# Kernel tuning notes

Hardware: AMD Instinct MI355X
Metric: run time of the kernel (lower is better)

## Reference

```python
import jax, jax.numpy as jnp
import numpy as np

B, S, HID = 1, 2048, 2048   # batch, block_size, hidden_dim
H, D = 16, 128              # num_heads, head_dim
WORLD_SIZE = 4
LOCAL_BLOCK_IDX = 3         # last rank: all kv blocks are causally visible


def setup_inputs() -> dict:
    key = jax.random.key(0)
    ks = jax.random.split(key, 5)
    w = lambda k: jax.random.normal(k, (H * D, HID), dtype=jnp.float32) * 0.02
    return {
        "hidden_states": jax.random.normal(ks[0], (B, S, HID), dtype=jnp.float32),
        "q_w": w(ks[1]), "q_b": jnp.zeros((H * D,), jnp.float32),
        "k_w": w(ks[2]), "k_b": jnp.zeros((H * D,), jnp.float32),
        "v_w": w(ks[3]), "v_b": jnp.zeros((H * D,), jnp.float32),
        "o_w": jax.random.normal(ks[4], (HID, H * D), dtype=jnp.float32) * 0.02,
        "o_b": jnp.zeros((HID,), jnp.float32),
        "world_size": WORLD_SIZE,
        "local_block_idx": LOCAL_BLOCK_IDX,
    }


def reference(hidden_states, q_w, q_b, k_w, k_b, v_w, v_b, o_w, o_b,
              world_size, local_block_idx):
    Bsz, Sq, _ = hidden_states.shape

    def proj(w, b):  # (B,S,HID) -> (B,H,S,D)
        return (hidden_states @ w.T + b).reshape(Bsz, Sq, H, D).transpose(0, 2, 1, 3)

    q, k, v = proj(q_w, q_b), proj(k_w, k_b), proj(v_w, v_b)
    scale = D ** -0.5

    # ring_send_recv is a local copy, so K/V are identical every ring step;
    # only the causal masking differs (triu mask on the diagonal block step).
    scores_base = jnp.einsum('bhqd,bhkd->bhqk', q, k) * scale
    tri = jnp.triu(jnp.ones((Sq, Sq), bool), k=1)
    scores_diag = jnp.where(tri, -jnp.inf, scores_base)

    out = jnp.zeros((Bsz, H, Sq, D), hidden_states.dtype)
    mx = jnp.full((Bsz, H, Sq, 1), -jnp.inf, hidden_states.dtype)
    se = jnp.zeros((Bsz, H, Sq, 1), hidden_states.dtype)

    for step in range(world_size):  # small fixed ring loop
        kv_idx = (local_block_idx - step) % world_size
        scores = scores_diag if kv_idx == local_block_idx else scores_base
        # OnlineSoftmax.update (faithful, including block-wise normalization)
        bm = scores.max(axis=-1, keepdims=True)
        nm = jnp.maximum(mx, bm)
        old_s = jnp.exp(mx - nm)
        new_s = jnp.exp(bm - nm)
        be = jnp.exp(scores - bm)
        bs = be.sum(axis=-1, keepdims=True)
        se = se * old_s + bs * new_s
        aw = be / (bs + 1e-8)
        bo = jnp.einsum('bhqk,bhkd->bhqd', aw, v)
        out = out * old_s + bo * new_s
        mx = nm

    out = out / (se + 1e-8)  # OnlineSoftmax.finalize
    out = out.transpose(0, 2, 1, 3).reshape(Bsz, Sq, H * D)
    return out @ o_w.T + o_b
```

## Files before the change

### kernel.cpp

```cpp
#include <hip/hip_runtime.h>
#include <hip/hip_bf16.h>
#include <stdint.h>
#include <stddef.h>


typedef __attribute__((ext_vector_type(8))) short bf16x8;
typedef __attribute__((ext_vector_type(4))) float f32x4;

#define MFMA_BF16(a, b, c) __builtin_amdgcn_mfma_f32_16x16x32_bf16((a), (b), (c), 0, 0, 0)

__device__ __forceinline__ void load16_lds(const void* g, void* l) {
  __builtin_amdgcn_global_load_lds((const __attribute__((address_space(1))) void*)g,
                                   (__attribute__((address_space(3))) void*)l,
                                   16, 0, 0);
}

__device__ __forceinline__ unsigned short f2bf(float x) {
  union { __hip_bfloat16 b; unsigned short u; } cv;
  cv.b = __float2bfloat16(x);
  return cv.u;
}

__global__ __launch_bounds__(256) void cvt_all(
    const float4* __restrict__ s0, const float4* __restrict__ s1,
    const float4* __restrict__ s2, const float4* __restrict__ s3,
    const float4* __restrict__ s4,
    ushort4* __restrict__ d0, ushort4* __restrict__ d1,
    ushort4* __restrict__ d2, ushort4* __restrict__ d3,
    ushort4* __restrict__ d4) {
  const int seg = blockIdx.x >> 12;
  const int i = ((blockIdx.x & 4095) << 8) + threadIdx.x;
  const float4* s = seg == 0 ? s0 : seg == 1 ? s1 : seg == 2 ? s2 : seg == 3 ? s3 : s4;
  ushort4* d = seg == 0 ? d0 : seg == 1 ? d1 : seg == 2 ? d2 : seg == 3 ? d3 : d4;
  float4 v = s[i];
  ushort4 o;
  o.x = f2bf(v.x); o.y = f2bf(v.y); o.z = f2bf(v.z); o.w = f2bf(v.w);
  d[i] = o;
}

__global__ __launch_bounds__(256) void gemm_qkv(
    const unsigned short* __restrict__ A, const unsigned short* __restrict__ Bt,
    const float* __restrict__ qb, const float* __restrict__ kb,
    const float* __restrict__ vb,
    unsigned short* __restrict__ Qo, unsigned short* __restrict__ Ko,
    unsigned short* __restrict__ Vt) {
  __shared__ __align__(16) unsigned short sA[128 * 64];
  __shared__ __align__(16) unsigned short sB[128 * 64];
  const int tid = threadIdx.x;
  const int wave = tid >> 6, lane = tid & 63;
  const int quad = lane >> 4, l16 = lane & 15;
  const int wr = wave >> 1, wc = wave & 1;
  const int m0 = blockIdx.y << 7, n0 = blockIdx.x << 7;

  f32x4 acc[4][4] = {};

  for (int k0 = 0; k0 < 2048; k0 += 64) {
    __syncthreads();
#pragma unroll
    for (int t = 0; t < 4; t++) {
      const int i = t * 4 + wave;
      const int idx = i * 64 + lane;
      const int row = idx >> 3;
      const int c = (idx & 7) ^ (row & 7);
      load16_lds(A + (size_t)(m0 + row) * 2048 + k0 + c * 8, &sA[i * 512]);
      load16_lds(Bt + (size_t)(n0 + row) * 2048 + k0 + c * 8, &sB[i * 512]);
    }
    __syncthreads();
#pragma unroll
    for (int ks = 0; ks < 2; ks++) {
      bf16x8 af[4], bfr[4];
#pragma unroll
      for (int i = 0; i < 4; i++) {
        const int cs = ((ks * 4 + quad) ^ (l16 & 7)) << 3;
        af[i] = *(const bf16x8*)&sA[(wr * 64 + i * 16 + l16) * 64 + cs];
        bfr[i] = *(const bf16x8*)&sB[(wc * 64 + i * 16 + l16) * 64 + cs];
      }
#pragma unroll
      for (int mi = 0; mi < 4; mi++)
#pragma unroll
        for (int ni = 0; ni < 4; ni++)
          acc[mi][ni] = MFMA_BF16(af[mi], bfr[ni], acc[mi][ni]);
    }
  }

#pragma unroll
  for (int mi = 0; mi < 4; mi++) {
    const int row = m0 + wr * 64 + mi * 16 + quad * 4;
#pragma unroll
    for (int ni = 0; ni < 4; ni++) {
      const int col = n0 + wc * 64 + ni * 16 + l16;
#pragma unroll
      for (int r = 0; r < 4; r++) {
        const float v = acc[mi][ni][r];
        const int rr = row + r;
        if (col < 2048) {
          const int hh = col >> 7, d = col & 127;
          Qo[((size_t)hh * 2048 + rr) * 128 + d] = f2bf(v + qb[col]);
        } else if (col < 4096) {
          const int f = col - 2048;
          const int hh = f >> 7, d = f & 127;
          Ko[((size_t)hh * 2048 + rr) * 128 + d] = f2bf(v + kb[f]);
        } else {
          const int f = col - 4096;
          const int hh = f >> 7, d = f & 127;
          Vt[((size_t)hh * 128 + d) * 2048 + rr] = f2bf(v + vb[f]);
        }
      }
    }
  }
}

__global__ __launch_bounds__(256) void attn_fwd(
    const unsigned short* __restrict__ Q, const unsigned short* __restrict__ K,
    const unsigned short* __restrict__ V,
    unsigned short* __restrict__ O,
    const int* __restrict__ wsp) {
  const int h = blockIdx.y;
  const int q0 = blockIdx.x << 6;
  const int tid = threadIdx.x;
  const int wave = tid >> 6, lane = tid & 63;
  const int quad = lane >> 4, l16 = lane & 15;

  __shared__ __align__(16) unsigned short sQ[64 * 128];
  __shared__ __align__(16) unsigned short sK[64 * 128];
  __shared__ __align__(16) unsigned short sV[128 * 64];
  __shared__ __align__(16) unsigned short sP[4][16 * 64];

  const unsigned short* Qh = Q + (size_t)h * 2048 * 128;
  const unsigned short* Kh = K + (size_t)h * 2048 * 128;
  const unsigned short* Vh = V + (size_t)h * 128 * 2048;
  unsigned short* sPw = sP[wave];

  for (int c = wave; c < 16; c += 4) {
    const int rowc = lane >> 4;
    const int row = c * 4 + rowc;
    const int blk = (lane & 15) ^ (row & 15);
    load16_lds(Qh + (size_t)(q0 + row) * 128 + blk * 8, &sQ[c * 512]);
  }
  __syncthreads();

  bf16x8 qf[4];
#pragma unroll
  for (int ds = 0; ds < 4; ds++)
    qf[ds] = *(const bf16x8*)&sQ[(wave * 16 + l16) * 128 + (((ds * 4 + quad) ^ l16) << 3)];

  float m1[4], l1[4], m2[4], l2[4];
  f32x4 o1[8], o2[8];
#pragma unroll
  for (int r = 0; r < 4; r++) { m1[r] = m2[r] = -3.0e38f; l1[r] = l2[r] = 0.f; }
#pragma unroll
  for (int j = 0; j < 8; j++) { o1[j] = f32x4{0.f, 0.f, 0.f, 0.f}; o2[j] = f32x4{0.f, 0.f, 0.f, 0.f}; }

  const float scale = 0.088388347648318447f;
  const int diag = q0 >> 6;

  auto update = [&](float (&m)[4], float (&l)[4], f32x4 (&o)[8],
                    const f32x4 (&sc)[4], bool masked, int k0) {
#pragma unroll
    for (int r = 0; r < 4; r++) {
      const int row = q0 + wave * 16 + quad * 4 + r;
      const int qr = quad * 4 + r;
      float s[4];
      float mx = -3.0e38f;
#pragma unroll
      for (int ni = 0; ni < 4; ni++) {
        float v = sc[ni][r] * scale;
        if (masked && (k0 + ni * 16 + l16 > row)) v = -3.0e38f;
        s[ni] = v;
        mx = fmaxf(mx, v);
      }
#pragma unroll
      for (int off = 1; off < 16; off <<= 1) mx = fmaxf(mx, __shfl_xor(mx, off));
      const float mn = fmaxf(m[r], mx);
      const float al = __expf(m[r] - mn);
      float rs = 0.f;
#pragma unroll
      for (int ni = 0; ni < 4; ni++) {
        const float p = __expf(s[ni] - mn);
        rs += p;
        const int pblk = ((ni * 2 + (l16 >> 3)) ^ (qr & 7));
        sPw[qr * 64 + pblk * 8 + (l16 & 7)] = f2bf(p);
      }
#pragma unroll
      for (int off = 1; off < 16; off <<= 1) rs += __shfl_xor(rs, off);
      l[r] = l[r] * al + rs;
      m[r] = mn;
#pragma unroll
      for (int j = 0; j < 8; j++) o[j][r] *= al;
    }
#pragma unroll
    for (int ks = 0; ks < 2; ks++) {
      const bf16x8 pf = *(const bf16x8*)&sPw[l16 * 64 + (((ks * 4 + quad) ^ (l16 & 7)) << 3)];
#pragma unroll
      for (int j = 0; j < 8; j++) {
        const bf16x8 vf =
            *(const bf16x8*)&sV[(j * 16 + l16) * 64 + (((ks * 4 + quad) ^ (l16 & 7)) << 3)];
        o[j] = MFMA_BF16(pf, vf, o[j]);
      }
    }
  };

  for (int kt = 0; kt < 32; kt++) {
    const int k0 = kt << 6;
    __syncthreads();
    for (int c = wave; c < 16; c += 4) {
      {
        const int rowc = lane >> 4;
        const int row = c * 4 + rowc;
        const int blk = (lane & 15) ^ (row & 15);
        load16_lds(Kh + (size_t)(k0 + row) * 128 + blk * 8, &sK[c * 512]);
      }
      {
        const int rowc = lane >> 3;
        const int row = c * 8 + rowc;
        const int blk = (lane & 7) ^ (rowc & 7);
        load16_lds(Vh + (size_t)row * 2048 + k0 + blk * 8, &sV[c * 512]);
      }
    }
    __syncthreads();

    f32x4 sc[4];
#pragma unroll
    for (int ni = 0; ni < 4; ni++) sc[ni] = f32x4{0.f, 0.f, 0.f, 0.f};
#pragma unroll
    for (int ds = 0; ds < 4; ds++) {
#pragma unroll
      for (int ni = 0; ni < 4; ni++) {
        const bf16x8 kf =
            *(const bf16x8*)&sK[(ni * 16 + l16) * 128 + (((ds * 4 + quad) ^ l16) << 3)];
        sc[ni] = MFMA_BF16(qf[ds], kf, sc[ni]);
      }
    }

    if (kt == diag) {
#pragma unroll
      for (int r = 0; r < 4; r++) { m1[r] = m2[r]; l1[r] = l2[r]; }
#pragma unroll
      for (int j = 0; j < 8; j++) o1[j] = o2[j];
      update(m1, l1, o1, sc, true, k0);
    }
    update(m2, l2, o2, sc, false, k0);
  }

  const float fws = (float)(wsp[0] - 1);
#pragma unroll
  for (int r = 0; r < 4; r++) {
    const int row = q0 + wave * 16 + quad * 4 + r;
    const float a = __expf(m1[r] - m2[r]);
    const float se = l1[r] * a + fws * l2[r];
    const float c1 = a / (l1[r] + 1e-8f);
    const float c2 = fws / (l2[r] + 1e-8f);
    const float inv = 1.0f / (se + 1e-8f);
#pragma unroll
    for (int j = 0; j < 8; j++) {
      const float ov = (o1[j][r] * c1 + o2[j][r] * c2) * inv;
      O[(size_t)row * 2048 + h * 128 + j * 16 + l16] = f2bf(ov);
    }
  }
}

__global__ __launch_bounds__(256) void gemm_o(
    const unsigned short* __restrict__ A, const unsigned short* __restrict__ Bt,
    const float* __restrict__ ob, float* __restrict__ Cout) {
  __shared__ __align__(16) unsigned short sA[64 * 64];
  __shared__ __align__(16) unsigned short sB[128 * 64];
  const int tid = threadIdx.x;
  const int wave = tid >> 6, lane = tid & 63;
  const int quad = lane >> 4, l16 = lane & 15;
  const int wm = wave >> 1, wn = wave & 1;
  const int m0 = blockIdx.y << 6, n0 = blockIdx.x << 7;

  f32x4 acc[2][4] = {};

  for (int k0 = 0; k0 < 2048; k0 += 64) {
    __syncthreads();
#pragma unroll
    for (int t = 0; t < 2; t++) {
      const int i = t * 4 + wave;
      const int idx = i * 64 + lane;
      const int row = idx >> 3;
      const int c = (idx & 7) ^ (row & 7);
      load16_lds(A + (size_t)(m0 + row) * 2048 + k0 + c * 8, &sA[i * 512]);
    }
#pragma unroll
    for (int t = 0; t < 4; t++) {
      const int i = t * 4 + wave;
      const int idx = i * 64 + lane;
      const int row = idx >> 3;
      const int c = (idx & 7) ^ (row & 7);
      load16_lds(Bt + (size_t)(n0 + row) * 2048 + k0 + c * 8, &sB[i * 512]);
    }
    __syncthreads();
#pragma unroll
    for (int ks = 0; ks < 2; ks++) {
      const int cs = ((ks * 4 + quad) ^ (l16 & 7)) << 3;
      bf16x8 af[2], bfr[4];
#pragma unroll
      for (int i = 0; i < 2; i++)
        af[i] = *(const bf16x8*)&sA[(wm * 32 + i * 16 + l16) * 64 + cs];
#pragma unroll
      for (int i = 0; i < 4; i++)
        bfr[i] = *(const bf16x8*)&sB[(wn * 64 + i * 16 + l16) * 64 + cs];
#pragma unroll
      for (int mi = 0; mi < 2; mi++)
#pragma unroll
        for (int ni = 0; ni < 4; ni++)
          acc[mi][ni] = MFMA_BF16(af[mi], bfr[ni], acc[mi][ni]);
    }
  }

#pragma unroll
  for (int mi = 0; mi < 2; mi++) {
    const int row = m0 + wm * 32 + mi * 16 + quad * 4;
#pragma unroll
    for (int ni = 0; ni < 4; ni++) {
      const int col = n0 + wn * 64 + ni * 16 + l16;
#pragma unroll
      for (int r = 0; r < 4; r++) {
        Cout[(size_t)(row + r) * 2048 + col] = acc[mi][ni][r] + ob[col];
      }
    }
  }
}

extern "C" void kernel_launch(void* const* d_in, const int* in_sizes, int n_in,
                              void* d_out, int out_size, void* d_ws, size_t ws_size,
                              hipStream_t stream) {
  (void)in_sizes; (void)n_in; (void)out_size; (void)ws_size;
  const float* hs = (const float*)d_in[0];
  const float* qw = (const float*)d_in[1];
  const float* qb = (const float*)d_in[2];
  const float* kw = (const float*)d_in[3];
  const float* kb = (const float*)d_in[4];
  const float* vw = (const float*)d_in[5];
  const float* vb = (const float*)d_in[6];
  const float* ow = (const float*)d_in[7];
  const float* ob = (const float*)d_in[8];
  const int* wsz = (const int*)d_in[9];

  char* w = (char*)d_ws;
  unsigned short* hsb  = (unsigned short*)(w + 0);
  unsigned short* wqkv = (unsigned short*)(w + 8388608);
  unsigned short* owb  = (unsigned short*)(w + 33554432);
  unsigned short* Qb_  = (unsigned short*)(w + 41943040);
  unsigned short* Kb_  = (unsigned short*)(w + 50331648);
  unsigned short* Vtb  = (unsigned short*)(w + 58720256);
  unsigned short* atb  = (unsigned short*)(w + 67108864);

  cvt_all<<<20480, 256, 0, stream>>>(
      (const float4*)hs, (const float4*)qw, (const float4*)kw, (const float4*)vw,
      (const float4*)ow,
      (ushort4*)hsb, (ushort4*)wqkv, (ushort4*)(wqkv + 4194304),
      (ushort4*)(wqkv + 8388608), (ushort4*)owb);

  gemm_qkv<<<dim3(48, 16), 256, 0, stream>>>(hsb, wqkv, qb, kb, vb, Qb_, Kb_, Vtb);
  attn_fwd<<<dim3(32, 16), 256, 0, stream>>>(Qb_, Kb_, Vtb, atb, wsz);
  gemm_o<<<dim3(16, 32), 256, 0, stream>>>(atb, owb, ob, (float*)d_out);
}
```

Before: 347.8 us.

## Transpose score MFMA so each lane owns one query row; fold scale into Q

The QK^T MFMA now swaps its operands and produces S^T. Each lane then holds all 16 scores of a single query row, so the row max and row sum need only two cross-lane shuffles instead of four shuffle steps for each of four rows. P is written to LDS as packed 4-element stores. The rescale factors are broadcast back to the output layout with __shfl. The softmax scale times log2(e) is folded into the Q projection epilogue so the attention loop can use exp2f without a per-score multiply. The cost is extra shuffles for the per-row broadcast of the rescale factors, and Q is rounded to bf16 after scaling, which slightly changes numerics.

```diff
diff --git a/kernel.cpp b/kernel.cpp
--- a/kernel.cpp
+++ b/kernel.cpp
@@ -83,6 +83,7 @@
     }
   }
 
+  const float qscale = 0.088388347648318447f * 1.4426950408889634f;
 #pragma unroll
   for (int mi = 0; mi < 4; mi++) {
     const int row = m0 + wr * 64 + mi * 16 + quad * 4;
@@ -95,7 +96,7 @@
         const int rr = row + r;
         if (col < 2048) {
           const int hh = col >> 7, d = col & 127;
-          Qo[((size_t)hh * 2048 + rr) * 128 + d] = f2bf(v + qb[col]);
+          Qo[((size_t)hh * 2048 + rr) * 128 + d] = f2bf((v + qb[col]) * qscale);
         } else if (col < 4096) {
           const int f = col - 2048;
           const int hh = f >> 7, d = f & 127;
@@ -144,49 +145,54 @@
   for (int ds = 0; ds < 4; ds++)
     qf[ds] = *(const bf16x8*)&sQ[(wave * 16 + l16) * 128 + (((ds * 4 + quad) ^ l16) << 3)];
 
-  float m1[4], l1[4], m2[4], l2[4];
+  float m1 = -3.0e38f, l1 = 0.f, m2 = -3.0e38f, l2 = 0.f;
   f32x4 o1[8], o2[8];
 #pragma unroll
-  for (int r = 0; r < 4; r++) { m1[r] = m2[r] = -3.0e38f; l1[r] = l2[r] = 0.f; }
-#pragma unroll
   for (int j = 0; j < 8; j++) { o1[j] = f32x4{0.f, 0.f, 0.f, 0.f}; o2[j] = f32x4{0.f, 0.f, 0.f, 0.f}; }
 
-  const float scale = 0.088388347648318447f;
   const int diag = q0 >> 6;
-
-  auto update = [&](float (&m)[4], float (&l)[4], f32x4 (&o)[8],
-                    const f32x4 (&sc)[4], bool masked, int k0) {
+  const int qg = q0 + wave * 16 + l16;
+
+  auto update = [&](float& m, float& l, f32x4 (&o)[8],
+                    const f32x4 (&st)[4], bool masked, int k0) {
+    float t[4][4];
+    float mx = -3.0e38f;
+#pragma unroll
+    for (int ni = 0; ni < 4; ni++)
+#pragma unroll
+      for (int r = 0; r < 4; r++) {
+        float v = st[ni][r];
+        if (masked && (k0 + ni * 16 + quad * 4 + r > qg)) v = -3.0e38f;
+        t[ni][r] = v;
+        mx = fmaxf(mx, v);
+      }
+    mx = fmaxf(mx, __shfl_xor(mx, 16));
+    mx = fmaxf(mx, __shfl_xor(mx, 32));
+    const float mn = fmaxf(m, mx);
+    const float al = exp2f(m - mn);
+    float rs = 0.f;
+#pragma unroll
+    for (int ni = 0; ni < 4; ni++) {
+      union { unsigned short u[4]; uint2 v; } pk;
+#pragma unroll
+      for (int r = 0; r < 4; r++) {
+        const float p = exp2f(t[ni][r] - mn);
+        rs += p;
+        pk.u[r] = f2bf(p);
+      }
+      const int off = l16 * 64 + (((ni * 2 + (quad >> 1)) ^ (l16 & 7)) << 3) + ((quad & 1) << 2);
+      *(uint2*)&sPw[off] = pk.v;
+    }
+    rs += __shfl_xor(rs, 16);
+    rs += __shfl_xor(rs, 32);
+    l = l * al + rs;
+    m = mn;
 #pragma unroll
     for (int r = 0; r < 4; r++) {
-      const int row = q0 + wave * 16 + quad * 4 + r;
-      const int qr = quad * 4 + r;
-      float s[4];
-      float mx = -3.0e38f;
-#pragma unroll
-      for (int ni = 0; ni < 4; ni++) {
-        float v = sc[ni][r] * scale;
-        if (masked && (k0 + ni * 16 + l16 > row)) v = -3.0e38f;
-        s[ni] = v;
-        mx = fmaxf(mx, v);
-      }
-#pragma unroll
-      for (int off = 1; off < 16; off <<= 1) mx = fmaxf(mx, __shfl_xor(mx, off));
-      const float mn = fmaxf(m[r], mx);
-      const float al = __expf(m[r] - mn);
-      float rs = 0.f;
-#pragma unroll
-      for (int ni = 0; ni < 4; ni++) {
-        const float p = __expf(s[ni] - mn);
-        rs += p;
-        const int pblk = ((ni * 2 + (l16 >> 3)) ^ (qr & 7));
-        sPw[qr * 64 + pblk * 8 + (l16 & 7)] = f2bf(p);
-      }
-#pragma unroll
-      for (int off = 1; off < 16; off <<= 1) rs += __shfl_xor(rs, off);
-      l[r] = l[r] * al + rs;
-      m[r] = mn;
-#pragma unroll
-      for (int j = 0; j < 8; j++) o[j][r] *= al;
+      const int src = (lane & 48) + ((lane >> 4) << 2) + r;
+      const float ab = __shfl(al, src);
+#pragma unroll
+      for (int j = 0; j < 8; j++) o[j][r] *= ab;
     }
 #pragma unroll
     for (int ks = 0; ks < 2; ks++) {
@@ -219,41 +225,43 @@
     }
     __syncthreads();
 
-    f32x4 sc[4];
-#pragma unroll
-    for (int ni = 0; ni < 4; ni++) sc[ni] = f32x4{0.f, 0.f, 0.f, 0.f};
+    f32x4 st[4];
+#pragma unroll
+    for (int ni = 0; ni < 4; ni++) st[ni] = f32x4{0.f, 0.f, 0.f, 0.f};
 #pragma unroll
     for (int ds = 0; ds < 4; ds++) {
 #pragma unroll
       for (int ni = 0; ni < 4; ni++) {
         const bf16x8 kf =
             *(const bf16x8*)&sK[(ni * 16 + l16) * 128 + (((ds * 4 + quad) ^ l16) << 3)];
-        sc[ni] = MFMA_BF16(qf[ds], kf, sc[ni]);
+        st[ni] = MFMA_BF16(kf, qf[ds], st[ni]);
       }
     }
 
     if (kt == diag) {
-#pragma unroll
-      for (int r = 0; r < 4; r++) { m1[r] = m2[r]; l1[r] = l2[r]; }
+      m1 = m2; l1 = l2;
 #pragma unroll
       for (int j = 0; j < 8; j++) o1[j] = o2[j];
-      update(m1, l1, o1, sc, true, k0);
-    }
-    update(m2, l2, o2, sc, false, k0);
+      update(m1, l1, o1, st, true, k0);
+    }
+    update(m2, l2, o2, st, false, k0);
   }
 
   const float fws = (float)(wsp[0] - 1);
+  const float a = exp2f(m1 - m2);
+  const float se = l1 * a + fws * l2;
+  const float inv = 1.0f / (se + 1e-8f);
+  const float f1 = (a / (l1 + 1e-8f)) * inv;
+  const float f2 = (fws / (l2 + 1e-8f)) * inv;
 #pragma unroll
   for (int r = 0; r < 4; r++) {
+    const int src = (lane & 48) + ((lane >> 4) << 2) + r;
+    const float f1b = __shfl(f1, src);
+    const float f2b = __shfl(f2, src);
     const int row = q0 + wave * 16 + quad * 4 + r;
-    const float a = __expf(m1[r] - m2[r]);
-    const float se = l1[r] * a + fws * l2[r];
-    const float c1 = a / (l1[r] + 1e-8f);
-    const float c2 = fws / (l2[r] + 1e-8f);
-    const float inv = 1.0f / (se + 1e-8f);
 #pragma unroll
     for (int j = 0; j < 8; j++) {
-      const float ov = (o1[j][r] * c1 + o2[j][r] * c2) * inv;
+      const float ov = o1[j][r] * f1b + o2[j][r] * f2b;
       O[(size_t)row * 2048 + h * 128 + j * 16 + l16] = f2bf(ov);
     }
   }
```

Result: faster. 334.7 us (-3.8%).
